# Kernel optimization log

Hardware: AMD Instinct MI355X
Metric: run time of the kernel (lower is better)

The kernel has to match this reference:

```python
import jax, jax.numpy as jnp
import numpy as np

EPS_SQUASH = 1e-6
EPS_BN = 1e-5
N_ITER = 3


def _squash(t, axis=-1):
    s = jnp.sum(t * t, axis=axis, keepdims=True)
    return s * t / ((1.0 + s) * jnp.sqrt(s + EPS_SQUASH))


def _conv(x, w, stride, pad):
    return jax.lax.conv_general_dilated(
        x, w, (stride, stride), ((pad, pad), (pad, pad)),
        dimension_numbers=('NCHW', 'OIHW', 'NCHW'))


def _bn_relu(x, g, b):
    # BatchNorm2d in training mode: batch statistics over (N,H,W), biased var
    m = jnp.mean(x, axis=(0, 2, 3), keepdims=True)
    v = jnp.var(x, axis=(0, 2, 3), keepdims=True)
    y = (x - m) / jnp.sqrt(v + EPS_BN) * g[None, :, None, None] + b[None, :, None, None]
    return jax.nn.relu(y)


def setup_inputs() -> dict:
    key = jax.random.key(0)
    ks = jax.random.split(key, 8)
    n = lambda k, shape, std: jax.random.normal(k, shape, jnp.float32) * std
    return dict(
        images=jax.random.normal(ks[0], (64, 3, 32, 32), jnp.float32),
        w1=n(ks[1], (48, 3, 3, 3), 0.1), g1=jnp.ones((48,), jnp.float32), b1=jnp.zeros((48,), jnp.float32),
        w2=n(ks[2], (96, 48, 3, 3), 0.1), g2=jnp.ones((96,), jnp.float32), b2=jnp.zeros((96,), jnp.float32),
        w3=n(ks[3], (192, 96, 3, 3), 0.1), g3=jnp.ones((192,), jnp.float32), b3=jnp.zeros((192,), jnp.float32),
        wp=n(ks[4], (192, 192, 3, 3), 0.1), bp=jnp.zeros((192,), jnp.float32),
        w_cc=n(ks[5], (144, 192, 12), 0.5),        # ConvCapsLayer weights, std=0.5 per source
        w_class=n(ks[6], (784, 10, 16, 12), 0.1),  # CapsLayer weights, std=0.1 per source
    )


def reference(images, w1, g1, b1, w2, g2, b2, w3, g3, b3, wp, bp, w_cc, w_class):
    B = images.shape[0]
    # conv stack: 32 -> 32 -> 16 -> 16
    x = _bn_relu(_conv(images, w1, 1, 1), g1, b1)
    x = _bn_relu(_conv(x, w2, 2, 1), g2, b2)
    x = _bn_relu(_conv(x, w3, 1, 1), g3, b3)
    # primary caps conv: 16 -> 7, 192 channels = 16 caps x 12 dim
    pc = _conv(x, wp, 2, 0) + bp[None, :, None, None]      # (B,192,7,7)
    u = _squash(pc.reshape(B, 784, 12))                    # (B,784,12), matches torch .view

    # ---- ConvCapsLayer (k=3, s=1, p=1) ----
    x4 = u.reshape(B, 192, 7, 7)
    xp = jnp.pad(x4, ((0, 0), (0, 0), (1, 1), (1, 1)))
    # F.unfold ordering: channel slowest, then (ki,kj), then spatial L row-major
    patches = jnp.stack([xp[:, :, i:i + 7, j:j + 7] for i in range(3) for j in range(3)], axis=2)  # (B,192,9,7,7)
    uu = patches.reshape(B, 192 * 9, 49).reshape(B, 49, 144, 12)  # faithful to torch .view reinterpretation
    u_hat = jnp.einsum('koi,btki->btko', w_cc, uu).reshape(B, 49, 144, 16, 12)
    b_log = jnp.zeros((B, 49, 144, 16, 1), jnp.float32)
    for r in range(N_ITER):
        c = jax.nn.softmax(b_log, axis=3)
        v = _squash(jnp.sum(c * u_hat, axis=2, keepdims=True))   # (B,49,1,16,12)
        if r < N_ITER - 1:
            b_log = b_log + jnp.sum(v * u_hat, axis=-1, keepdims=True)
    u2 = v.reshape(B, 784, 12)

    # ---- Class CapsLayer ----
    u_hat2 = jnp.einsum('nodi,bni->bnod', w_class, u2)           # (B,784,10,16)
    b2l = jnp.zeros((B, 784, 10, 1), jnp.float32)
    for r in range(N_ITER):
        c = jax.nn.softmax(b2l, axis=2)
        v = _squash(jnp.sum(c * u_hat2, axis=1, keepdims=True))  # (B,1,10,16)
        if r < N_ITER - 1:
            b2l = b2l + jnp.sum(v * u_hat2, axis=-1, keepdims=True)
    return v.reshape(B, 10, 16)
```

## Files before the change

### kernel.cpp

```cpp
#include <hip/hip_runtime.h>
#include <hip/hip_bf16.h>

typedef __attribute__((ext_vector_type(4))) short short4v;
typedef __attribute__((ext_vector_type(8))) short short8v;
typedef __attribute__((ext_vector_type(16))) float f32x16;

union frag8 { short8v v8; struct { short4v lo, hi; } p; };

__device__ __forceinline__ unsigned short f2bf(float v) {
  unsigned u = __float_as_uint(v);
  unsigned r = u + 0x7fffu + ((u >> 16) & 1u);
  return (unsigned short)(r >> 16);
}
__device__ __forceinline__ float bf2f(unsigned short h) {
  return __uint_as_float(((unsigned)h) << 16);
}

__global__ __launch_bounds__(192) void conv1_fused(const float* __restrict__ images,
                                                   const float* __restrict__ w1,
                                                   float* __restrict__ out) {
  int b = blockIdx.x >> 5, h = blockIdx.x & 31;
  __shared__ __align__(16) float lin[3][3][36];
  int tid = threadIdx.x;
  for (int e = tid; e < 324; e += 192) {
    int ci = e / 108, rem = e % 108, ki = rem / 36, wi = rem % 36;
    int row = h + ki - 1, col = wi - 1;
    float v = 0.f;
    if (row >= 0 && row < 32 && col >= 0 && col < 32)
      v = images[((size_t)(b*3 + ci)*32 + row)*32 + col];
    lin[ci][ki][wi] = v;
  }
  int co = tid >> 2, ws = tid & 3;
  float wr[27];
  #pragma unroll
  for (int j = 0; j < 27; ++j) wr[j] = w1[co*27 + j];
  __syncthreads();
  float o[8];
  #pragma unroll
  for (int j = 0; j < 8; ++j) o[j] = 0.f;
  #pragma unroll
  for (int ci = 0; ci < 3; ++ci)
    #pragma unroll
    for (int ki = 0; ki < 3; ++ki) {
      float4 q0 = *(const float4*)&lin[ci][ki][ws*8];
      float4 q1 = *(const float4*)&lin[ci][ki][ws*8+4];
      float4 q2 = *(const float4*)&lin[ci][ki][ws*8+8];
      float r[12] = {q0.x,q0.y,q0.z,q0.w,q1.x,q1.y,q1.z,q1.w,q2.x,q2.y,q2.z,q2.w};
      #pragma unroll
      for (int kj = 0; kj < 3; ++kj) {
        float wv = wr[(ci*3+ki)*3+kj];
        #pragma unroll
        for (int j = 0; j < 8; ++j) o[j] = fmaf(r[j+kj], wv, o[j]);
      }
    }
  float* dst = out + (((size_t)(b*48+co)*32 + h)*32 + ws*8);
  *(float4*)dst       = make_float4(o[0],o[1],o[2],o[3]);
  *(float4*)(dst + 4) = make_float4(o[4],o[5],o[6],o[7]);
}

__device__ __forceinline__ void split_one(const float* w, unsigned short* wh,
                                          unsigned short* wl, int CI, int i) {
  int K = CI*9;
  int co = i / K, rem = i % K, tap = rem / CI, ci = rem % CI;
  float v = w[(co*CI + ci)*9 + tap];
  unsigned short h = f2bf(v);
  wh[i] = h;
  wl[i] = f2bf(v - bf2f(h));
}
__global__ void split_w_all(const float* __restrict__ w2, const float* __restrict__ w3,
                            const float* __restrict__ wp,
                            unsigned short* wh2, unsigned short* wl2,
                            unsigned short* wh3, unsigned short* wl3,
                            unsigned short* whp, unsigned short* wlp) {
  int i = blockIdx.x*256 + threadIdx.x;
  if (i < 41472) split_one(w2, wh2, wl2, 48, i);
  else if (i < 207360) split_one(w3, wh3, wl3, 96, i - 41472);
  else if (i < 539136) split_one(wp, whp, wlp, 192, i - 207360);
}

template<int C,int H,int W,int P>
__global__ void bn_split_nhwc(const float* __restrict__ in, const float* __restrict__ sc,
                              unsigned short* __restrict__ xh, unsigned short* __restrict__ xl) {
  constexpr int HP = H + 2*P, WP = W + 2*P;
  int b = blockIdx.x / HP, hp = blockIdx.x % HP;
  int h = hp - P;
  for (int e = threadIdx.x; e < WP*C; e += 256) {
    int wp = e / C, c = e % C;
    int w = wp - P;
    float v = 0.f;
    if (h >= 0 && h < H && w >= 0 && w < W) {
      v = in[((size_t)(b*C + c)*H + h)*W + w];
      v = fmaf(v, sc[c*2], sc[c*2+1]);
      v = v > 0.f ? v : 0.f;
    }
    unsigned short hh = f2bf(v);
    size_t o = ((size_t)(b*HP + hp)*WP + wp)*C + c;
    xh[o] = hh;
    xl[o] = f2bf(v - bf2f(hh));
  }
}

template<int CI,int HIP,int WIP,int HO,int WO,int STR,int SPLITK>
__global__ __launch_bounds__(256,4) void conv_mfma(
    const unsigned short* __restrict__ xh, const unsigned short* __restrict__ xl,
    const unsigned short* __restrict__ wh, const unsigned short* __restrict__ wl,
    float* __restrict__ part, int CO, int B) {
  constexpr int K = CI*9, NSP = HO*WO, KCH = K/SPLITK, LDA = 36;
  const int NTOT = B*NSP;
  const int m0 = blockIdx.x*64, n0 = blockIdx.y*128, ks = blockIdx.z;
  __shared__ unsigned short Ah[64*LDA], Al[64*LDA], Bh[128*LDA], Bl[128*LDA];
  const int tid = threadIdx.x, lane = tid & 63, wid = tid >> 6;
  const int wm = wid >> 1, wn = wid & 1;
  const int arow = tid >> 2, ak0 = (tid & 3)*8;
  const bool aok = (m0 + arow) < CO;
  const size_t abase = (size_t)(m0 + arow)*K;
  int brow[2], bk0[2];
  size_t bbase[2];
  #pragma unroll
  for (int i = 0; i < 2; ++i) {
    int e = tid + i*256;
    brow[i] = e >> 2; bk0[i] = (e & 3)*8;
    int nn = n0 + brow[i]; if (nn > NTOT-1) nn = NTOT-1;
    int bb = nn / NSP, sp = nn % NSP;
    int ho = sp / WO, wo = sp % WO;
    bbase[i] = ((size_t)bb*HIP + ho*STR)*WIP + wo*STR;
  }
  f32x16 acc0 = (f32x16)0.f, acc1 = (f32x16)0.f;
  const int kBeg = ks*KCH, kEnd = kBeg + KCH;
  for (int kc = kBeg; kc < kEnd; kc += 32) {
    const int kLim = (kEnd - kc) < 32 ? (kEnd - kc) : 32;
    {
      frag8 vh, vl;
      vh.v8 = (short8v)(short)0; vl.v8 = (short8v)(short)0;
      if (aok && ak0 < kLim) {
        size_t off = abase + kc + ak0;
        vh.v8 = *(const short8v*)(wh + off);
        vl.v8 = *(const short8v*)(wl + off);
      }
      int lo_ = arow*LDA + ak0;
      *(short4v*)(Ah + lo_) = vh.p.lo; *(short4v*)(Ah + lo_ + 4) = vh.p.hi;
      *(short4v*)(Al + lo_) = vl.p.lo; *(short4v*)(Al + lo_ + 4) = vl.p.hi;
    }
    #pragma unroll
    for (int i = 0; i < 2; ++i) {
      frag8 vh, vl;
      vh.v8 = (short8v)(short)0; vl.v8 = (short8v)(short)0;
      if (bk0[i] < kLim) {
        int kg = kc + bk0[i];
        int tap = kg / CI, ci0 = kg - tap*CI;
        int dh = tap / 3, dw = tap - dh*3;
        size_t off = (bbase[i] + (size_t)dh*WIP + dw)*CI + ci0;
        vh.v8 = *(const short8v*)(xh + off);
        vl.v8 = *(const short8v*)(xl + off);
      }
      int lo_ = brow[i]*LDA + bk0[i];
      *(short4v*)(Bh + lo_) = vh.p.lo; *(short4v*)(Bh + lo_ + 4) = vh.p.hi;
      *(short4v*)(Bl + lo_) = vl.p.lo; *(short4v*)(Bl + lo_ + 4) = vl.p.hi;
    }
    __syncthreads();
    #pragma unroll
    for (int kst = 0; kst < 2; ++kst) {
      const int kb = kst*16 + 8*(lane >> 5);
      const int ar = wm*32 + (lane & 31);
      frag8 ah, al;
      { int o = ar*LDA + kb;
        ah.p.lo = *(const short4v*)(Ah + o); ah.p.hi = *(const short4v*)(Ah + o + 4);
        al.p.lo = *(const short4v*)(Al + o); al.p.hi = *(const short4v*)(Al + o + 4); }
      const int br = wn*64 + (lane & 31);
      frag8 bh0, bl0, bh1, bl1;
      { int o = br*LDA + kb;
        bh0.p.lo = *(const short4v*)(Bh + o); bh0.p.hi = *(const short4v*)(Bh + o + 4);
        bl0.p.lo = *(const short4v*)(Bl + o); bl0.p.hi = *(const short4v*)(Bl + o + 4); }
      { int o = (br+32)*LDA + kb;
        bh1.p.lo = *(const short4v*)(Bh + o); bh1.p.hi = *(const short4v*)(Bh + o + 4);
        bl1.p.lo = *(const short4v*)(Bl + o); bl1.p.hi = *(const short4v*)(Bl + o + 4); }
      acc0 = __builtin_amdgcn_mfma_f32_32x32x16_bf16(ah.v8, bh0.v8, acc0, 0, 0, 0);
      acc0 = __builtin_amdgcn_mfma_f32_32x32x16_bf16(ah.v8, bl0.v8, acc0, 0, 0, 0);
      acc0 = __builtin_amdgcn_mfma_f32_32x32x16_bf16(al.v8, bh0.v8, acc0, 0, 0, 0);
      acc1 = __builtin_amdgcn_mfma_f32_32x32x16_bf16(ah.v8, bh1.v8, acc1, 0, 0, 0);
      acc1 = __builtin_amdgcn_mfma_f32_32x32x16_bf16(ah.v8, bl1.v8, acc1, 0, 0, 0);
      acc1 = __builtin_amdgcn_mfma_f32_32x32x16_bf16(al.v8, bh1.v8, acc1, 0, 0, 0);
    }
    __syncthreads();
  }
  #pragma unroll
  for (int ns = 0; ns < 2; ++ns) {
    f32x16 a = ns ? acc1 : acc0;
    #pragma unroll
    for (int r = 0; r < 16; ++r) {
      int row = (r & 3) + 8*(r >> 2) + 4*(lane >> 5);
      int m = m0 + wm*32 + row;
      int n = n0 + wn*64 + ns*32 + (lane & 31);
      if (m < CO && n < NTOT) {
        if (SPLITK == 1) {
          int b = n / NSP, sp = n % NSP;
          part[((size_t)b*CO + m)*NSP + sp] = a[r];
        } else {
          part[((size_t)ks*CO + m)*NTOT + n] = a[r];
        }
      }
    }
  }
}

template<int CO,int NSP,int SPLITK,bool BIAS,bool STATS>
__global__ void splitk_reduce(const float* __restrict__ part, const float* __restrict__ bias,
                              float* __restrict__ out, float* __restrict__ stats, int B) {
  const int NTOT = B*NSP;
  int i = blockIdx.x*256 + threadIdx.x;
  bool valid = i < CO*NTOT;
  float s = 0.f;
  if (valid) {
    int co = i / NTOT, n = i % NTOT;
    #pragma unroll
    for (int ks = 0; ks < SPLITK; ++ks) s += part[(size_t)(ks*CO + co)*NTOT + n];
    if (BIAS) s += bias[co];
    int b = n / NSP, sp = n % NSP;
    out[((size_t)b*CO + co)*NSP + sp] = s;
  }
  if (STATS) {
    float sum = valid ? s : 0.f, sq = valid ? s*s : 0.f;
    #pragma unroll
    for (int off = 32; off; off >>= 1) {
      sum += __shfl_down(sum, off, 64);
      sq  += __shfl_down(sq,  off, 64);
    }
    __shared__ float ls[2][4];
    int lane = threadIdx.x & 63, wv = threadIdx.x >> 6;
    if (lane == 0) { ls[0][wv] = sum; ls[1][wv] = sq; }
    __syncthreads();
    if (threadIdx.x == 0) {
      float S = 0.f, Q = 0.f;
      #pragma unroll
      for (int j = 0; j < 4; ++j) { S += ls[0][j]; Q += ls[1][j]; }
      int bpc = NTOT/256;
      int co = blockIdx.x / bpc, slice = blockIdx.x % bpc;
      stats[(co*bpc + slice)*2 + 0] = S;
      stats[(co*bpc + slice)*2 + 1] = Q;
    }
  }
}

template<int C,int HW,int SLICES>
__global__ void bn_partial(const float* __restrict__ x, float* __restrict__ part, int B) {
  int c = blockIdx.x / SLICES, s = blockIdx.x % SLICES;
  int bpp = B / SLICES;
  float sum = 0.f, sq = 0.f;
  for (int b = s*bpp; b < (s+1)*bpp; ++b) {
    const float* p = x + ((size_t)b*C + c)*HW;
    for (int i = threadIdx.x; i < HW; i += blockDim.x) {
      float v = p[i]; sum += v; sq += v*v;
    }
  }
  #pragma unroll
  for (int off = 32; off; off >>= 1) {
    sum += __shfl_down(sum, off, 64);
    sq  += __shfl_down(sq,  off, 64);
  }
  __shared__ float ls[2][4];
  int lane = threadIdx.x & 63, wv = threadIdx.x >> 6;
  if (lane == 0) { ls[0][wv] = sum; ls[1][wv] = sq; }
  __syncthreads();
  if (threadIdx.x == 0) {
    float S = 0.f, Q = 0.f;
    #pragma unroll
    for (int i = 0; i < 4; ++i) { S += ls[0][i]; Q += ls[1][i]; }
    part[(c*SLICES+s)*2+0] = S; part[(c*SLICES+s)*2+1] = Q;
  }
}

template<int C,int SLICES>
__global__ void bn_final(const float* __restrict__ part, const float* __restrict__ g,
                         const float* __restrict__ bta, float* __restrict__ sc, int NHW) {
  int c = blockIdx.x*blockDim.x + threadIdx.x;
  if (c >= C) return;
  float S = 0.f, Q = 0.f;
  for (int s = 0; s < SLICES; ++s) { S += part[(c*SLICES+s)*2]; Q += part[(c*SLICES+s)*2+1]; }
  float m = S / NHW, v = Q / NHW - m*m;
  float inv = rsqrtf(v + 1e-5f);
  float a = g[c] * inv;
  sc[c*2] = a; sc[c*2+1] = bta[c] - m*a;
}

__global__ void squash_pc(float* __restrict__ pc, int ncaps) {
  int i = blockIdx.x*blockDim.x + threadIdx.x;
  if (i >= ncaps) return;
  float* p = pc + (size_t)i*12;
  float v[12]; float s = 0.f;
  #pragma unroll
  for (int d = 0; d < 12; ++d) { v[d] = p[d]; s += v[d]*v[d]; }
  float sc = s / ((1.f + s)*sqrtf(s + 1e-6f));
  #pragma unroll
  for (int d = 0; d < 12; ++d) p[d] = v[d]*sc;
}

__global__ void uu_gather(const float* __restrict__ sq, float* __restrict__ uu, int B) {
  int idx = blockIdx.x*blockDim.x + threadIdx.x;
  int total = B*49*144*12;
  if (idx >= total) return;
  int ii = idx % 12; int t0 = idx / 12;
  int kk = t0 % 144; t0 /= 144;
  int tt = t0 % 49;  int b = t0 / 49;
  int f = tt*1728 + kk*12 + ii;
  int c = f / 441; int r = f - c*441;
  int k = r / 49;  int sp = r - k*49;
  int y = sp / 7, x = sp - y*7;
  int iy = y + k/3 - 1, ix = x + (k%3) - 1;
  float val = 0.f;
  if (iy >= 0 && iy < 7 && ix >= 0 && ix < 7)
    val = sq[((size_t)(b*192 + c)*7 + iy)*7 + ix];
  uu[idx] = val;
}

__global__ __launch_bounds__(192) void cc_einsum2(const float* __restrict__ uu,
                                                  const float* __restrict__ wcc,
                                                  __hip_bfloat16* __restrict__ uhat,
                                                  int row0, int nrows) {
  int k  = blockIdx.x;
  int m0 = blockIdx.y * 64;
  int o = threadIdx.x;
  const float4* wp4 = (const float4*)(wcc + ((size_t)k*192 + o)*12);
  float4 w0 = wp4[0], w1 = wp4[1], w2 = wp4[2];
  int mmax = nrows - m0; if (mmax > 64) mmax = 64;
  #pragma unroll 2
  for (int m = 0; m < mmax; ++m) {
    const float4* ar = (const float4*)(uu + ((size_t)(row0+m0+m)*144 + k)*12);
    float4 a0 = ar[0], a1 = ar[1], a2 = ar[2];
    float acc = a0.x*w0.x + a0.y*w0.y + a0.z*w0.z + a0.w*w0.w
              + a1.x*w1.x + a1.y*w1.y + a1.z*w1.z + a1.w*w1.w
              + a2.x*w2.x + a2.y*w2.y + a2.z*w2.z + a2.w*w2.w;
    uhat[((size_t)(m0+m)*144 + k)*192 + o] = __float2bfloat16(acc);
  }
}

__global__ __launch_bounds__(512) void cc_route(const __hip_bfloat16* __restrict__ uhat,
                                                float* __restrict__ u2, int rowOff) {
  const int row = blockIdx.x;
  const unsigned short* __restrict__ uh = (const unsigned short*)uhat + (size_t)row*27648;
  __shared__ float blog[144*16];
  __shared__ float cc[144*16];
  __shared__ float sv8[8][192];
  __shared__ float sv0[192];
  __shared__ float svs[192];
  const int tid = threadIdx.x;
  for (int i = tid; i < 2304; i += 512) blog[i] = 0.f;
  __syncthreads();
  for (int r = 0; r < 3; ++r) {
    if (tid < 144) {
      float mx = -1e30f;
      #pragma unroll
      for (int o = 0; o < 16; ++o) mx = fmaxf(mx, blog[tid*16+o]);
      float e[16]; float ssum = 0.f;
      #pragma unroll
      for (int o = 0; o < 16; ++o) { e[o] = __expf(blog[tid*16+o]-mx); ssum += e[o]; }
      float inv = 1.f/ssum;
      #pragma unroll
      for (int o = 0; o < 16; ++o) cc[tid*16+o] = e[o]*inv;
    }
    __syncthreads();
    if (tid < 384) {
      int q = tid / 48, o4 = tid % 48;
      int oc = o4 / 3;
      const unsigned short* up = uh + o4*4;
      float a0 = 0.f, a1 = 0.f, a2 = 0.f, a3 = 0.f;
      #pragma unroll 6
      for (int k = q*18; k < q*18+18; ++k) {
        uint2 u = *(const uint2*)(up + k*192);
        float c = cc[k*16 + oc];
        a0 = fmaf(c, bf2f((unsigned short)(u.x & 0xffff)), a0);
        a1 = fmaf(c, bf2f((unsigned short)(u.x >> 16)),   a1);
        a2 = fmaf(c, bf2f((unsigned short)(u.y & 0xffff)), a2);
        a3 = fmaf(c, bf2f((unsigned short)(u.y >> 16)),   a3);
      }
      sv8[q][o4*4+0] = a0; sv8[q][o4*4+1] = a1;
      sv8[q][o4*4+2] = a2; sv8[q][o4*4+3] = a3;
    }
    __syncthreads();
    if (tid < 192) {
      float s = 0.f;
      #pragma unroll
      for (int q = 0; q < 8; ++q) s += sv8[q][tid];
      sv0[tid] = s;
    }
    __syncthreads();
    if (tid < 192) {
      int oc = tid / 12;
      float nrm = 0.f;
      #pragma unroll
      for (int d = 0; d < 12; ++d) { float v = sv0[oc*12+d]; nrm += v*v; }
      float sc = nrm / ((1.f + nrm)*sqrtf(nrm + 1e-6f));
      svs[tid] = sv0[tid]*sc;
    }
    __syncthreads();
    if (r < 2) {
      for (int p = tid; p < 2304; p += 512) {
        int k = p >> 4, oc = p & 15;
        const unsigned short* up = uh + k*192 + oc*12;
        uint2 u0 = *(const uint2*)(up);
        uint2 u1 = *(const uint2*)(up + 4);
        uint2 u2v = *(const uint2*)(up + 8);
        const float* vp = svs + oc*12;
        float dot = 0.f;
        dot = fmaf(vp[0],  bf2f((unsigned short)(u0.x & 0xffff)), dot);
        dot = fmaf(vp[1],  bf2f((unsigned short)(u0.x >> 16)),    dot);
        dot = fmaf(vp[2],  bf2f((unsigned short)(u0.y & 0xffff)), dot);
        dot = fmaf(vp[3],  bf2f((unsigned short)(u0.y >> 16)),    dot);
        dot = fmaf(vp[4],  bf2f((unsigned short)(u1.x & 0xffff)), dot);
        dot = fmaf(vp[5],  bf2f((unsigned short)(u1.x >> 16)),    dot);
        dot = fmaf(vp[6],  bf2f((unsigned short)(u1.y & 0xffff)), dot);
        dot = fmaf(vp[7],  bf2f((unsigned short)(u1.y >> 16)),    dot);
        dot = fmaf(vp[8],  bf2f((unsigned short)(u2v.x & 0xffff)), dot);
        dot = fmaf(vp[9],  bf2f((unsigned short)(u2v.x >> 16)),    dot);
        dot = fmaf(vp[10], bf2f((unsigned short)(u2v.y & 0xffff)), dot);
        dot = fmaf(vp[11], bf2f((unsigned short)(u2v.y >> 16)),    dot);
        blog[p] += dot;
      }
      __syncthreads();
    }
  }
  if (tid < 192) u2[((size_t)(rowOff + row))*192 + tid] = svs[tid];
}

__global__ void class_einsum(const float* __restrict__ u2, const float* __restrict__ wcl,
                             unsigned short* __restrict__ uhat2, int B) {
  int n = blockIdx.x;
  __shared__ float u2l[64][12];
  int tid = threadIdx.x;
  for (int e = tid; e < 64*12; e += 320) {
    int b = e / 12, i = e % 12;
    u2l[b][i] = u2[(size_t)b*9408 + n*12 + i];
  }
  __syncthreads();
  int od = tid % 160, bh = tid / 160;
  int o = od >> 4, d = od & 15;
  float w[12];
  #pragma unroll
  for (int i = 0; i < 12; ++i) w[i] = wcl[(size_t)n*1920 + o*192 + d*12 + i];
  for (int b = bh*32; b < bh*32+32; ++b) {
    float acc = 0.f;
    #pragma unroll
    for (int i = 0; i < 12; ++i) acc = fmaf(w[i], u2l[b][i], acc);
    uhat2[((size_t)b*784 + n)*160 + od] = f2bf(acc);
  }
}

template<int MODE>
__global__ __launch_bounds__(256) void cls_pass(const unsigned short* __restrict__ uh2b,
                                                const float* __restrict__ vprev,
                                                float* __restrict__ b2l,
                                                float* __restrict__ cpart) {
  const int b = blockIdx.x, sl = blockIdx.y;
  const int tid = threadIdx.x, lane = tid & 63, wv = tid >> 6;
  const int nl = lane >> 4, d = lane & 15;
  float v[10];
  if (MODE != 0) {
    #pragma unroll
    for (int o = 0; o < 10; ++o) v[o] = vprev[b*160 + o*16 + d];
  }
  float sacc[10];
  #pragma unroll
  for (int o = 0; o < 10; ++o) sacc[o] = 0.f;
  for (int step = 0; step < 7; ++step) {
    const int n = sl*112 + step*16 + wv*4 + nl;
    const unsigned short* up = uh2b + ((size_t)b*784 + n)*160 + d;
    float u[10];
    #pragma unroll
    for (int o = 0; o < 10; ++o) u[o] = bf2f(up[o*16]);
    if (MODE == 0) {
      #pragma unroll
      for (int o = 0; o < 10; ++o) sacc[o] += u[o];
    } else {
      float bb[10];
      #pragma unroll
      for (int o = 0; o < 10; ++o) {
        float t = v[o]*u[o];
        #pragma unroll
        for (int off = 8; off; off >>= 1) t += __shfl_xor(t, off, 16);
        bb[o] = t;
      }
      if (MODE == 2) {
        #pragma unroll
        for (int o = 0; o < 10; ++o) bb[o] += b2l[((size_t)b*784 + n)*10 + o];
      }
      if (MODE == 1 && d < 10) b2l[((size_t)b*784 + n)*10 + d] = bb[d];
      float mx = bb[0];
      #pragma unroll
      for (int o = 1; o < 10; ++o) mx = fmaxf(mx, bb[o]);
      float es = 0.f;
      #pragma unroll
      for (int o = 0; o < 10; ++o) { bb[o] = __expf(bb[o]-mx); es += bb[o]; }
      float inv = 1.f/es;
      #pragma unroll
      for (int o = 0; o < 10; ++o) sacc[o] = fmaf(bb[o]*inv, u[o], sacc[o]);
    }
  }
  #pragma unroll
  for (int o = 0; o < 10; ++o) {
    sacc[o] += __shfl_xor(sacc[o], 16, 64);
    sacc[o] += __shfl_xor(sacc[o], 32, 64);
  }
  __shared__ float red[4][160];
  if (lane < 16) {
    #pragma unroll
    for (int o = 0; o < 10; ++o) red[wv][o*16 + d] = sacc[o];
  }
  __syncthreads();
  if (tid < 160) {
    float s = red[0][tid] + red[1][tid] + red[2][tid] + red[3][tid];
    cpart[((size_t)b*7 + sl)*160 + tid] = s;
  }
}

__global__ __launch_bounds__(160) void cls_finish(const float* __restrict__ cpart,
                                                  float* __restrict__ vout, float fac) {
  int b = blockIdx.x, od = threadIdx.x;
  float s = 0.f;
  #pragma unroll
  for (int sl = 0; sl < 7; ++sl) s += cpart[((size_t)b*7 + sl)*160 + od];
  s *= fac;
  float nrm = s*s;
  #pragma unroll
  for (int off = 8; off; off >>= 1) nrm += __shfl_xor(nrm, off, 16);
  float sc = nrm / ((1.f + nrm)*sqrtf(nrm + 1e-6f));
  vout[(size_t)b*160 + od] = s*sc;
}

extern "C" void kernel_launch(void* const* d_in, const int* in_sizes, int n_in,
                              void* d_out, int out_size, void* d_ws, size_t ws_size,
                              hipStream_t stream) {
  const float* images = (const float*)d_in[0];
  const float* w1  = (const float*)d_in[1];
  const float* g1  = (const float*)d_in[2];
  const float* b1  = (const float*)d_in[3];
  const float* w2  = (const float*)d_in[4];
  const float* g2  = (const float*)d_in[5];
  const float* b2  = (const float*)d_in[6];
  const float* w3  = (const float*)d_in[7];
  const float* g3  = (const float*)d_in[8];
  const float* b3  = (const float*)d_in[9];
  const float* wp  = (const float*)d_in[10];
  const float* bp  = (const float*)d_in[11];
  const float* wcc = (const float*)d_in[12];
  const float* wcl = (const float*)d_in[13];
  float* out = (float*)d_out;
  float* ws  = (float*)d_ws;

  float* t1    = ws + 0;
  float* t2    = ws + 3145728;
  float* t3    = ws + 4718592;
  float* pc    = ws + 7864320;
  float* uu    = ws + 8466432;
  float* u2b   = ws + 13885440;
  unsigned short* uh2b = (unsigned short*)(ws + 14487552);
  float* b2l   = ws + 22515712;
  float* scrC  = ws + 23017472;
  float* v2    = ws + 23519232;
  float* spart = ws + 23529472;
  float* ssc1  = ws + 23532544;
  float* ssc2  = ws + 23532640;
  float* ssc3  = ws + 23532832;
  float* U     = ws + 23533312;
  __hip_bfloat16* uhc = (__hip_bfloat16*)(ws + 34371328);

  unsigned short* wh2 = (unsigned short*)(uu + 0);
  unsigned short* wl2 = (unsigned short*)(uu + 20736);
  unsigned short* wh3 = (unsigned short*)(uu + 41472);
  unsigned short* wl3 = (unsigned short*)(uu + 124416);
  unsigned short* whp = (unsigned short*)(uu + 207360);
  unsigned short* wlp = (unsigned short*)(uu + 373248);

  unsigned short* x2h = (unsigned short*)(U + 0);
  unsigned short* x2l = (unsigned short*)(U + 1775616);
  float*          part2 = U + 3551232;
  unsigned short* x3h = (unsigned short*)(U + 0);
  unsigned short* x3l = (unsigned short*)(U + 995328);
  unsigned short* xph = (unsigned short*)(U + 0);
  unsigned short* xpl = (unsigned short*)(U + 1572864);
  float*          partp = U + 3145728;

  const int B = 64;

  split_w_all<<<2106,256,0,stream>>>(w2, w3, wp, wh2, wl2, wh3, wl3, whp, wlp);

  conv1_fused<<<2048,192,0,stream>>>(images, w1, t1);
  bn_partial<48,1024,8><<<48*8,256,0,stream>>>(t1, spart, B);
  bn_final<48,8><<<1,64,0,stream>>>(spart, g1, b1, ssc1, 65536);

  bn_split_nhwc<48,32,32,1><<<64*34,256,0,stream>>>(t1, ssc1, x2h, x2l);
  conv_mfma<48,34,34,16,16,2,3><<<dim3(2,128,3),256,0,stream>>>(x2h, x2l, wh2, wl2, part2, 96, B);
  splitk_reduce<96,256,3,false,true><<<6144,256,0,stream>>>(part2, nullptr, t2, scrC, B);
  bn_final<96,64><<<1,128,0,stream>>>(scrC, g2, b2, ssc2, 16384);

  bn_split_nhwc<96,16,16,1><<<64*18,256,0,stream>>>(t2, ssc2, x3h, x3l);
  conv_mfma<96,18,18,16,16,1,1><<<dim3(3,128,1),256,0,stream>>>(x3h, x3l, wh3, wl3, t3, 192, B);
  bn_partial<192,256,8><<<192*8,256,0,stream>>>(t3, spart, B);
  bn_final<192,8><<<1,192,0,stream>>>(spart, g3, b3, ssc3, 16384);

  bn_split_nhwc<192,16,16,0><<<64*16,256,0,stream>>>(t3, ssc3, xph, xpl);
  conv_mfma<192,16,16,7,7,2,8><<<dim3(3,25,8),256,0,stream>>>(xph, xpl, whp, wlp, partp, 192, B);
  splitk_reduce<192,49,8,true,false><<<2352,256,0,stream>>>(partp, bp, pc, nullptr, B);
  squash_pc<<<196,256,0,stream>>>(pc, 50176);

  uu_gather<<<21168,256,0,stream>>>(pc, uu, B);
  for (int cb = 0; cb < 2; ++cb) {
    cc_einsum2<<<dim3(144,25),192,0,stream>>>(uu, wcc, uhc, cb*1568, 1568);
    cc_route<<<1568,512,0,stream>>>(uhc, u2b, cb*1568);
  }
  class_einsum<<<784,320,0,stream>>>(u2b, wcl, uh2b, B);
  cls_pass<0><<<dim3(64,7),256,0,stream>>>(uh2b, v2, b2l, scrC);
  cls_finish<<<64,160,0,stream>>>(scrC, v2, 0.1f);
  cls_pass<1><<<dim3(64,7),256,0,stream>>>(uh2b, v2, b2l, scrC);
  cls_finish<<<64,160,0,stream>>>(scrC, v2, 1.0f);
  cls_pass<2><<<dim3(64,7),256,0,stream>>>(uh2b, v2, b2l, scrC);
  cls_finish<<<64,160,0,stream>>>(scrC, out, 1.0f);
  (void)in_sizes; (void)n_in; (void)out_size; (void)ws_size;
}
```

Baseline: 410.7 us.

## Restructure conv-caps routing to keep logits in registers and fuse agreement with softmax

The ConvCaps routing kernel now runs with 256 threads, each owning one output capsule for 9 input capsules. The routing logits stay in registers, and softmax over the 16 outputs uses 16-lane shuffles. The agreement update, softmax and weighted sum now happen in one pass over u_hat per iteration, where before there were separate passes with shared-memory logits and coupling tables. The first iteration uses uniform coefficients as a plain sum scaled by 1/16. This cuts global reads of u_hat and block barriers, at the cost of more registers and a 16-way shared-memory reduction.

```diff
diff --git a/kernel.cpp b/kernel.cpp
--- a/kernel.cpp
+++ b/kernel.cpp
@@ -333,92 +333,83 @@
   }
 }
 
-__global__ __launch_bounds__(512) void cc_route(const __hip_bfloat16* __restrict__ uhat,
+__global__ __launch_bounds__(256) void cc_route(const __hip_bfloat16* __restrict__ uhat,
                                                 float* __restrict__ u2, int rowOff) {
   const int row = blockIdx.x;
   const unsigned short* __restrict__ uh = (const unsigned short*)uhat + (size_t)row*27648;
-  __shared__ float blog[144*16];
-  __shared__ float cc[144*16];
-  __shared__ float sv8[8][192];
-  __shared__ float sv0[192];
-  __shared__ float svs[192];
+  __shared__ float red[16][192];
+  __shared__ float sraw[192];
+  __shared__ float vsh[192];
   const int tid = threadIdx.x;
-  for (int i = tid; i < 2304; i += 512) blog[i] = 0.f;
-  __syncthreads();
+  const int g = tid >> 4, oc = tid & 15;
+  const unsigned short* __restrict__ ubase = uh + oc*12;
+  float blog[9];
+  #pragma unroll
+  for (int j = 0; j < 9; ++j) blog[j] = 0.f;
+  float sacc[12];
+
   for (int r = 0; r < 3; ++r) {
-    if (tid < 144) {
-      float mx = -1e30f;
-      #pragma unroll
-      for (int o = 0; o < 16; ++o) mx = fmaxf(mx, blog[tid*16+o]);
-      float e[16]; float ssum = 0.f;
-      #pragma unroll
-      for (int o = 0; o < 16; ++o) { e[o] = __expf(blog[tid*16+o]-mx); ssum += e[o]; }
-      float inv = 1.f/ssum;
-      #pragma unroll
-      for (int o = 0; o < 16; ++o) cc[tid*16+o] = e[o]*inv;
-    }
-    __syncthreads();
-    if (tid < 384) {
-      int q = tid / 48, o4 = tid % 48;
-      int oc = o4 / 3;
-      const unsigned short* up = uh + o4*4;
-      float a0 = 0.f, a1 = 0.f, a2 = 0.f, a3 = 0.f;
-      #pragma unroll 6
-      for (int k = q*18; k < q*18+18; ++k) {
-        uint2 u = *(const uint2*)(up + k*192);
-        float c = cc[k*16 + oc];
-        a0 = fmaf(c, bf2f((unsigned short)(u.x & 0xffff)), a0);
-        a1 = fmaf(c, bf2f((unsigned short)(u.x >> 16)),   a1);
-        a2 = fmaf(c, bf2f((unsigned short)(u.y & 0xffff)), a2);
-        a3 = fmaf(c, bf2f((unsigned short)(u.y >> 16)),   a3);
+    #pragma unroll
+    for (int d = 0; d < 12; ++d) sacc[d] = 0.f;
+    float vq[12];
+    if (r > 0) {
+      #pragma unroll
+      for (int d = 0; d < 12; ++d) vq[d] = vsh[oc*12 + d];
+    }
+    for (int j = 0; j < 9; ++j) {
+      const unsigned short* up = ubase + (g + 16*j)*192;
+      uint2 q0 = *(const uint2*)up;
+      uint2 q1 = *(const uint2*)(up + 4);
+      uint2 q2 = *(const uint2*)(up + 8);
+      float uf[12];
+      uf[0] = bf2f((unsigned short)(q0.x & 0xffff)); uf[1] = bf2f((unsigned short)(q0.x >> 16));
+      uf[2] = bf2f((unsigned short)(q0.y & 0xffff)); uf[3] = bf2f((unsigned short)(q0.y >> 16));
+      uf[4] = bf2f((unsigned short)(q1.x & 0xffff)); uf[5] = bf2f((unsigned short)(q1.x >> 16));
+      uf[6] = bf2f((unsigned short)(q1.y & 0xffff)); uf[7] = bf2f((unsigned short)(q1.y >> 16));
+      uf[8] = bf2f((unsigned short)(q2.x & 0xffff)); uf[9] = bf2f((unsigned short)(q2.x >> 16));
+      uf[10] = bf2f((unsigned short)(q2.y & 0xffff)); uf[11] = bf2f((unsigned short)(q2.y >> 16));
+      if (r == 0) {
+        #pragma unroll
+        for (int d = 0; d < 12; ++d) sacc[d] += uf[d];
+      } else {
+        float dot = 0.f;
+        #pragma unroll
+        for (int d = 0; d < 12; ++d) dot = fmaf(vq[d], uf[d], dot);
+        blog[j] += dot;
+        float mx = blog[j];
+        #pragma unroll
+        for (int off = 1; off < 16; off <<= 1) mx = fmaxf(mx, __shfl_xor(mx, off, 16));
+        float e = __expf(blog[j] - mx);
+        float es = e;
+        #pragma unroll
+        for (int off = 1; off < 16; off <<= 1) es += __shfl_xor(es, off, 16);
+        float c = e / es;
+        #pragma unroll
+        for (int d = 0; d < 12; ++d) sacc[d] = fmaf(c, uf[d], sacc[d]);
       }
-      sv8[q][o4*4+0] = a0; sv8[q][o4*4+1] = a1;
-      sv8[q][o4*4+2] = a2; sv8[q][o4*4+3] = a3;
-    }
+    }
+    #pragma unroll
+    for (int d = 0; d < 12; ++d) red[g][oc*12 + d] = sacc[d];
     __syncthreads();
     if (tid < 192) {
       float s = 0.f;
       #pragma unroll
-      for (int q = 0; q < 8; ++q) s += sv8[q][tid];
-      sv0[tid] = s;
+      for (int q = 0; q < 16; ++q) s += red[q][tid];
+      if (r == 0) s *= 0.0625f;
+      sraw[tid] = s;
     }
     __syncthreads();
     if (tid < 192) {
-      int oc = tid / 12;
+      int qc = tid / 12;
       float nrm = 0.f;
       #pragma unroll
-      for (int d = 0; d < 12; ++d) { float v = sv0[oc*12+d]; nrm += v*v; }
+      for (int d = 0; d < 12; ++d) { float v = sraw[qc*12 + d]; nrm += v*v; }
       float sc = nrm / ((1.f + nrm)*sqrtf(nrm + 1e-6f));
-      svs[tid] = sv0[tid]*sc;
+      vsh[tid] = sraw[tid]*sc;
     }
     __syncthreads();
-    if (r < 2) {
-      for (int p = tid; p < 2304; p += 512) {
-        int k = p >> 4, oc = p & 15;
-        const unsigned short* up = uh + k*192 + oc*12;
-        uint2 u0 = *(const uint2*)(up);
-        uint2 u1 = *(const uint2*)(up + 4);
-        uint2 u2v = *(const uint2*)(up + 8);
-        const float* vp = svs + oc*12;
-        float dot = 0.f;
-        dot = fmaf(vp[0],  bf2f((unsigned short)(u0.x & 0xffff)), dot);
-        dot = fmaf(vp[1],  bf2f((unsigned short)(u0.x >> 16)),    dot);
-        dot = fmaf(vp[2],  bf2f((unsigned short)(u0.y & 0xffff)), dot);
-        dot = fmaf(vp[3],  bf2f((unsigned short)(u0.y >> 16)),    dot);
-        dot = fmaf(vp[4],  bf2f((unsigned short)(u1.x & 0xffff)), dot);
-        dot = fmaf(vp[5],  bf2f((unsigned short)(u1.x >> 16)),    dot);
-        dot = fmaf(vp[6],  bf2f((unsigned short)(u1.y & 0xffff)), dot);
-        dot = fmaf(vp[7],  bf2f((unsigned short)(u1.y >> 16)),    dot);
-        dot = fmaf(vp[8],  bf2f((unsigned short)(u2v.x & 0xffff)), dot);
-        dot = fmaf(vp[9],  bf2f((unsigned short)(u2v.x >> 16)),    dot);
-        dot = fmaf(vp[10], bf2f((unsigned short)(u2v.y & 0xffff)), dot);
-        dot = fmaf(vp[11], bf2f((unsigned short)(u2v.y >> 16)),    dot);
-        blog[p] += dot;
-      }
-      __syncthreads();
-    }
-  }
-  if (tid < 192) u2[((size_t)(rowOff + row))*192 + tid] = svs[tid];
+  }
+  if (tid < 192) u2[((size_t)(rowOff + row))*192 + tid] = vsh[tid];
 }
 
 __global__ void class_einsum(const float* __restrict__ u2, const float* __restrict__ wcl,
@@ -604,7 +595,7 @@
   uu_gather<<<21168,256,0,stream>>>(pc, uu, B);
   for (int cb = 0; cb < 2; ++cb) {
     cc_einsum2<<<dim3(144,25),192,0,stream>>>(uu, wcc, uhc, cb*1568, 1568);
-    cc_route<<<1568,512,0,stream>>>(uhc, u2b, cb*1568);
+    cc_route<<<1568,256,0,stream>>>(uhc, u2b, cb*1568);
   }
   class_einsum<<<784,320,0,stream>>>(u2b, wcl, uh2b, B);
   cls_pass<0><<<dim3(64,7),256,0,stream>>>(uh2b, v2, b2l, scrC);
```

After: 399.0 us. -2.8%, faster.
